# Optimization experiments

Hardware: AMD Instinct MI355X
Metric: run time of the kernel (lower is better)

## Reference

```python
import jax, jax.numpy as jnp
import numpy as np

DRUG_DIM, PROT_DIM, HIDDEN_DIM, OUTPUT_DIM = 128, 128, 256, 256


def setup_inputs() -> dict:
    key = jax.random.key(0)
    ks = jax.random.split(key, 7)
    B, n_d, n_p = 8, 64, 1024
    s = lambda d: 1.0 / np.sqrt(d)
    return {
        "X_d": jax.random.normal(ks[0], (B, n_d, DRUG_DIM), dtype=jnp.float32),
        "X_p": jax.random.normal(ks[1], (B, n_p, PROT_DIM), dtype=jnp.float32),
        # nn.Linear(in, out) weights have shape (out, in); we store transposed (in, out)
        "W_d": jax.random.uniform(ks[2], (DRUG_DIM, HIDDEN_DIM), jnp.float32, -s(DRUG_DIM), s(DRUG_DIM)),
        "W_p": jax.random.uniform(ks[3], (PROT_DIM, HIDDEN_DIM), jnp.float32, -s(PROT_DIM), s(PROT_DIM)),
        "W_a": jax.random.uniform(ks[4], (DRUG_DIM, OUTPUT_DIM), jnp.float32, -s(DRUG_DIM), s(DRUG_DIM)),
        "W_b": jax.random.uniform(ks[5], (PROT_DIM, OUTPUT_DIM), jnp.float32, -s(PROT_DIM), s(PROT_DIM)),
        "w_score": jax.random.uniform(ks[6], (HIDDEN_DIM,), jnp.float32, -s(HIDDEN_DIM), s(HIDDEN_DIM)),
    }


def reference(X_d, X_p, W_d, W_p, W_a, W_b, w_score):
    # Projections: (B, n_d, H), (B, n_p, H), (B, n_d, O), (B, n_p, O)
    hd = jnp.einsum("bik,kh->bih", X_d, W_d)
    hp = jnp.einsum("bjk,kh->bjh", X_p, W_p)
    fd = jnp.einsum("bik,ko->bio", X_d, W_a)
    fp = jnp.einsum("bjk,ko->bjo", X_p, W_b)

    # N_ij = tanh(hd_i + hp_j): (B, n_d, n_p, H); scores = N @ w_score
    N = jnp.tanh(hd[:, :, None, :] + hp[:, None, :, :])
    scores = jnp.einsum("bijh,h->bij", N, w_score)
    A = jax.nn.softmax(scores, axis=-1)  # softmax over protein dim

    # f_ij = tanh(fd_i + fp_j): (B, n_d, n_p, O)
    f = jnp.tanh(fd[:, :, None, :] + fp[:, None, :, :])
    X_int = jnp.einsum("bij,bijo->bo", A, f)  # sum over i and j
    return X_int
```

## Files before the change

### kernel.cpp

```cpp
#include <hip/hip_runtime.h>

#define NB   8
#define ND   64
#define NP   1024
#define KDIM 128
#define HID  256
#define OUTD 256
#define CSC  2.885390081777927f
#define PSTR 1048

typedef __attribute__((ext_vector_type(8))) short  bf16x8;
typedef __attribute__((ext_vector_type(4))) float  f32x4;


__device__ __forceinline__ ushort f2bf(float f) {
    unsigned u = __float_as_uint(f);
    return (ushort)((u + 0x7FFFu + ((u >> 16) & 1u)) >> 16);
}

__global__ __launch_bounds__(256) void k_cast(
    const float* __restrict__ Xd, const float* __restrict__ Xp,
    const float* __restrict__ Wd, const float* __restrict__ Wa,
    const float* __restrict__ Wp, const float* __restrict__ Wb,
    ushort* __restrict__ Xdbf, ushort* __restrict__ Xpbf,
    ushort* __restrict__ WdT, ushort* __restrict__ WaT,
    ushort* __restrict__ WpT, ushort* __restrict__ WbT) {
    int blk = blockIdx.x, t = threadIdx.x;
    if (blk < 1024) {
        size_t i = ((size_t)blk << 10) + ((size_t)t << 2);
        float4 v = *(const float4*)(Xp + i);
        ushort4 o; o.x = f2bf(v.x); o.y = f2bf(v.y); o.z = f2bf(v.z); o.w = f2bf(v.w);
        *(ushort4*)(Xpbf + i) = o;
    } else if (blk < 1088) {
        size_t i = ((size_t)(blk - 1024) << 10) + ((size_t)t << 2);
        float4 v = *(const float4*)(Xd + i);
        ushort4 o; o.x = f2bf(v.x); o.y = f2bf(v.y); o.z = f2bf(v.z); o.w = f2bf(v.w);
        *(ushort4*)(Xdbf + i) = o;
    } else {
        int r = blk - 1088, mat = r >> 5;
        const float* W = (mat == 0) ? Wd : (mat == 1) ? Wa : (mat == 2) ? Wp : Wb;
        ushort* WT = (mat == 0) ? WdT : (mat == 1) ? WaT : (mat == 2) ? WpT : WbT;
        int o0 = ((r & 31) << 10) + (t << 2);
        int n = o0 >> 7, k0 = o0 & 127;
        ushort4 o;
        o.x = f2bf(W[(k0 + 0) * HID + n]);
        o.y = f2bf(W[(k0 + 1) * HID + n]);
        o.z = f2bf(W[(k0 + 2) * HID + n]);
        o.w = f2bf(W[(k0 + 3) * HID + n]);
        *(ushort4*)(WT + o0) = o;
    }
}

__global__ __launch_bounds__(256) void k_proj_mfma(
    const ushort* __restrict__ Xpbf, const ushort* __restrict__ Xdbf,
    const ushort* __restrict__ WdT, const ushort* __restrict__ WaT,
    const ushort* __restrict__ WpT, const ushort* __restrict__ WbT,
    float* __restrict__ Ehd, float* __restrict__ Efd,
    float* __restrict__ EhpT, float* __restrict__ Efp) {
    int blk = blockIdx.x, t = threadIdx.x;
    const ushort *A, *B;
    float* out; size_t obase; int ostride, am0, bn0;
    if (blk < 512) {
        int mt = blk >> 2, nt = blk & 3;
        A = Xpbf; am0 = mt * 64; B = WbT; bn0 = nt * 64;
        out = Efp; obase = (size_t)am0 * HID + bn0; ostride = HID;
    } else if (blk < 1024) {
        int r = blk - 512, b = r >> 6, rr = r & 63;
        int mt = rr >> 4, nt = rr & 15;
        A = WpT; am0 = mt * 64;
        B = Xpbf + (size_t)b * NP * KDIM; bn0 = nt * 64;
        out = EhpT; obase = ((size_t)(b * 256 + am0)) * NP + bn0; ostride = NP;
    } else if (blk < 1056) {
        int r = blk - 1024; int mt = r >> 2, nt = r & 3;
        A = Xdbf; am0 = mt * 64; B = WdT; bn0 = nt * 64;
        out = Ehd; obase = (size_t)am0 * HID + bn0; ostride = HID;
    } else {
        int r = blk - 1056; int mt = r >> 2, nt = r & 3;
        A = Xdbf; am0 = mt * 64; B = WaT; bn0 = nt * 64;
        out = Efd; obase = (size_t)am0 * HID + bn0; ostride = HID;
    }
    int l = t & 63, w = t >> 6;
    int wm = (w >> 1) << 5, wn = (w & 1) << 5;
    int lr = l & 15, lk = (l >> 4) << 3;
    const ushort* Ab = A + (size_t)(am0 + wm + lr) * KDIM + lk;
    const ushort* Bb = B + (size_t)(bn0 + wn + lr) * KDIM + lk;

    bf16x8 af[2][4], bfr[2][4];
#pragma unroll
    for (int f = 0; f < 2; ++f)
#pragma unroll
        for (int ks = 0; ks < 4; ++ks) {
            af[f][ks]  = *(const bf16x8*)(Ab + (size_t)(f << 4) * KDIM + (ks << 5));
            bfr[f][ks] = *(const bf16x8*)(Bb + (size_t)(f << 4) * KDIM + (ks << 5));
        }

    f32x4 acc[2][2];
#pragma unroll
    for (int mf = 0; mf < 2; ++mf)
#pragma unroll
        for (int nf = 0; nf < 2; ++nf) acc[mf][nf] = (f32x4){0.f, 0.f, 0.f, 0.f};
#pragma unroll
    for (int ks = 0; ks < 4; ++ks)
#pragma unroll
        for (int mf = 0; mf < 2; ++mf)
#pragma unroll
            for (int nf = 0; nf < 2; ++nf)
                acc[mf][nf] = __builtin_amdgcn_mfma_f32_16x16x32_bf16(
                    af[mf][ks], bfr[nf][ks], acc[mf][nf], 0, 0, 0);

#pragma unroll
    for (int mf = 0; mf < 2; ++mf)
#pragma unroll
        for (int nf = 0; nf < 2; ++nf)
#pragma unroll
            for (int r = 0; r < 4; ++r) {
                int m = wm + (mf << 4) + ((l >> 4) << 2) + r;
                int n = wn + (nf << 4) + (l & 15);
                out[obase + (size_t)m * ostride + n] =
                    __builtin_amdgcn_exp2f(acc[mf][nf][r] * CSC);
            }
}

__global__ __launch_bounds__(1024) void k_fused(
    const float* __restrict__ Ehd, const float* __restrict__ EhpT,
    const float* __restrict__ Efd, const float* __restrict__ Efp,
    const float* __restrict__ wsc, float* __restrict__ part) {
    int blk = blockIdx.x;
    int b = blk & 7, pair = blk >> 3;
    int row0 = b * ND + pair * 2;
    int t = threadIdx.x;

    __shared__ float2 hrow[256];
    __shared__ float  w2s[256];
    __shared__ float2 a2[1024];
    __shared__ float  sred[8 * PSTR];
    __shared__ float  wsum0[16], wsum1[16];

    if (t < 256) {
        hrow[t] = make_float2(Ehd[((size_t)row0 << 8) + t],
                              Ehd[((size_t)(row0 + 1) << 8) + t]);
        w2s[t] = -2.0f * wsc[t];
    }
    __syncthreads();

    {
        int jq = t & 255, hq = t >> 8;
        const float* pB = EhpT + ((size_t)((b << 8) + (hq << 6))) * NP + (jq << 2);
        float a00 = 0, a01 = 0, a02 = 0, a03 = 0;
        float a10 = 0, a11 = 0, a12 = 0, a13 = 0;
        float4 pc = *(const float4*)(pB);
        float4 pn = *(const float4*)(pB + NP);
#pragma unroll
        for (int hh = 0; hh < 64; ++hh) {
            float4 pf = pc;
            if (hh + 2 < 64) pf = *(const float4*)(pB + (size_t)(hh + 2) * NP);
            int h = (hq << 6) + hh;
            float2 hv = hrow[h];
            float wv = w2s[h];
            a00 = fmaf(wv, __builtin_amdgcn_rcpf(fmaf(hv.x, pc.x, 1.f)), a00);
            a01 = fmaf(wv, __builtin_amdgcn_rcpf(fmaf(hv.x, pc.y, 1.f)), a01);
            a02 = fmaf(wv, __builtin_amdgcn_rcpf(fmaf(hv.x, pc.z, 1.f)), a02);
            a03 = fmaf(wv, __builtin_amdgcn_rcpf(fmaf(hv.x, pc.w, 1.f)), a03);
            a10 = fmaf(wv, __builtin_amdgcn_rcpf(fmaf(hv.y, pc.x, 1.f)), a10);
            a11 = fmaf(wv, __builtin_amdgcn_rcpf(fmaf(hv.y, pc.y, 1.f)), a11);
            a12 = fmaf(wv, __builtin_amdgcn_rcpf(fmaf(hv.y, pc.z, 1.f)), a12);
            a13 = fmaf(wv, __builtin_amdgcn_rcpf(fmaf(hv.y, pc.w, 1.f)), a13);
            pc = pn; pn = pf;
        }
        int base = (hq << 8) + jq;
        sred[0 * PSTR + base] = a00;  sred[1 * PSTR + base] = a01;
        sred[2 * PSTR + base] = a02;  sred[3 * PSTR + base] = a03;
        sred[4 * PSTR + base] = a10;  sred[5 * PSTR + base] = a11;
        sred[6 * PSTR + base] = a12;  sred[7 * PSTR + base] = a13;
    }
    __syncthreads();

    {
        int jq2 = t >> 2, c = t & 3;
        const float* p0 = sred + c * PSTR + jq2;
        const float* p1 = sred + (4 + c) * PSTR + jq2;
        float sc0 = (p0[0] + p0[256]) + (p0[512] + p0[768]);
        float sc1 = (p1[0] + p1[256]) + (p1[512] + p1[768]);
        const float L2E = 1.4426950408889634f;
        float e0 = __builtin_amdgcn_exp2f(sc0 * L2E);
        float e1 = __builtin_amdgcn_exp2f(sc1 * L2E);
        float s0 = e0, s1 = e1;
#pragma unroll
        for (int off = 32; off > 0; off >>= 1) {
            s0 += __shfl_xor(s0, off, 64);
            s1 += __shfl_xor(s1, off, 64);
        }
        if ((t & 63) == 0) { wsum0[t >> 6] = s0; wsum1[t >> 6] = s1; }
        __syncthreads();
        float tot0 = 0.f, tot1 = 0.f;
#pragma unroll
        for (int w = 0; w < 16; ++w) { tot0 += wsum0[w]; tot1 += wsum1[w]; }
        float sn0 = -2.0f * __builtin_amdgcn_rcpf(tot0);
        float sn1 = -2.0f * __builtin_amdgcn_rcpf(tot1);
        a2[t] = make_float2(e0 * sn0, e1 * sn1);
    }
    __syncthreads();

    {
        int oq = t & 63, jg = t >> 6;
        int o0 = oq << 2;
        float4 fd0 = *(const float4*)(Efd + ((size_t)row0 << 8) + o0);
        float4 fd1 = *(const float4*)(Efd + ((size_t)(row0 + 1) << 8) + o0);
        const float* fpB = Efp + ((size_t)(b * NP + (jg << 6)) << 8) + o0;
        float b00 = 0, b01 = 0, b02 = 0, b03 = 0;
        float b10 = 0, b11 = 0, b12 = 0, b13 = 0;
        float4 fc = *(const float4*)(fpB);
        float4 fn = *(const float4*)(fpB + 256);
#pragma unroll
        for (int jj = 0; jj < 64; ++jj) {
            float4 ff = fc;
            if (jj + 2 < 64) ff = *(const float4*)(fpB + ((size_t)(jj + 2) << 8));
            float2 av = a2[(jg << 6) + jj];
            b00 = fmaf(av.x, __builtin_amdgcn_rcpf(fmaf(fd0.x, fc.x, 1.f)), b00);
            b01 = fmaf(av.x, __builtin_amdgcn_rcpf(fmaf(fd0.y, fc.y, 1.f)), b01);
            b02 = fmaf(av.x, __builtin_amdgcn_rcpf(fmaf(fd0.z, fc.z, 1.f)), b02);
            b03 = fmaf(av.x, __builtin_amdgcn_rcpf(fmaf(fd0.w, fc.w, 1.f)), b03);
            b10 = fmaf(av.y, __builtin_amdgcn_rcpf(fmaf(fd1.x, fc.x, 1.f)), b10);
            b11 = fmaf(av.y, __builtin_amdgcn_rcpf(fmaf(fd1.y, fc.y, 1.f)), b11);
            b12 = fmaf(av.y, __builtin_amdgcn_rcpf(fmaf(fd1.z, fc.z, 1.f)), b12);
            b13 = fmaf(av.y, __builtin_amdgcn_rcpf(fmaf(fd1.w, fc.w, 1.f)), b13);
            fc = fn; fn = ff;
        }
        __syncthreads();
        int base = (jg << 6) + oq;
        sred[0 * PSTR + base] = b00;  sred[1 * PSTR + base] = b01;
        sred[2 * PSTR + base] = b02;  sred[3 * PSTR + base] = b03;
        sred[4 * PSTR + base] = b10;  sred[5 * PSTR + base] = b11;
        sred[6 * PSTR + base] = b12;  sred[7 * PSTR + base] = b13;
    }
    __syncthreads();

    if (t < 512) {
        int r = t >> 8, o = t & 255;
        int oq2 = o >> 2, c2 = o & 3;
        const float* pk = sred + (r * 4 + c2) * PSTR + oq2;
        float s = 0.f;
#pragma unroll
        for (int g = 0; g < 16; ++g) s += pk[g << 6];
        part[((size_t)((b << 6) + (pair << 1) + r) << 8) + o] = s;
    }
}

__global__ __launch_bounds__(256) void k_reduce(
    const float* __restrict__ part, float* __restrict__ out) {
    int b = blockIdx.x, t = threadIdx.x;
    float s = 64.0f;
#pragma unroll 8
    for (int i = 0; i < 64; ++i)
        s += part[((size_t)((b << 6) + i) << 8) + t];
    out[(b << 8) + t] = s;
}

extern "C" void kernel_launch(void* const* d_in, const int* in_sizes, int n_in,
                              void* d_out, int out_size, void* d_ws, size_t ws_size,
                              hipStream_t stream) {
    const float* Xd  = (const float*)d_in[0];
    const float* Xp  = (const float*)d_in[1];
    const float* Wd  = (const float*)d_in[2];
    const float* Wp  = (const float*)d_in[3];
    const float* Wa  = (const float*)d_in[4];
    const float* Wb  = (const float*)d_in[5];
    const float* wsc = (const float*)d_in[6];
    float* out = (float*)d_out;

    float* ws = (float*)d_ws;
    float* Ehd  = ws;
    float* Efd  = Ehd + NB * ND * HID;
    float* EhpT = Efd + NB * ND * OUTD;
    float* Efp  = EhpT + NB * NP * HID;
    float* stage = Efp + NB * NP * OUTD;
    ushort* Xpbf = (ushort*)stage;
    ushort* Xdbf = Xpbf + NB * NP * KDIM;
    ushort* WdT  = Xdbf + 65536;
    ushort* WaT  = WdT + 32768;
    ushort* WpT  = WaT + 32768;
    ushort* WbT  = WpT + 32768;
    float* part  = stage;

    k_cast     <<<1216, 256, 0, stream>>>(Xd, Xp, Wd, Wa, Wp, Wb,
                                          Xdbf, Xpbf, WdT, WaT, WpT, WbT);
    k_proj_mfma<<<1088, 256, 0, stream>>>(Xpbf, Xdbf, WdT, WaT, WpT, WbT,
                                          Ehd, Efd, EhpT, Efp);
    k_fused    <<<256, 1024, 0, stream>>>(Ehd, EhpT, Efd, Efp, wsc, part);
    k_reduce   <<<NB, 256, 0, stream>>>(part, out);
}
```

Baseline: 63.41 us.

## Stage hp/fp tiles into LDS with double-buffered async global_load_lds

Both main loops in the fused kernel now copy 32 KB chunks of the transposed hp and the fp projections into a two-slot LDS buffer using global_load_lds, instead of each thread streaming its own global loads through registers. While one chunk is being computed on, the next is prefetched, and the hd row and score weight are packed into one float4 table. The aim is to hide global/L2 latency and take load traffic out of the register file. In exchange it adds 64 extra block barriers, about 64 KB more LDS, and depends on the compiler inserting correct waits for the async LDS loads.

```diff
diff --git a/kernel.cpp b/kernel.cpp
--- a/kernel.cpp
+++ b/kernel.cpp
@@ -17,6 +17,10 @@
     unsigned u = __float_as_uint(f);
     return (ushort)((u + 0x7FFFu + ((u >> 16) & 1u)) >> 16);
 }
+
+#define GLD16(g, l) __builtin_amdgcn_global_load_lds(                        \
+    (const __attribute__((address_space(1))) void*)(g),                      \
+    (__attribute__((address_space(3))) void*)(l), 16, 0, 0)
 
 __global__ __launch_bounds__(256) void k_cast(
     const float* __restrict__ Xd, const float* __restrict__ Xp,
@@ -130,49 +134,59 @@
     int row0 = b * ND + pair * 2;
     int t = threadIdx.x;
 
-    __shared__ float2 hrow[256];
-    __shared__ float  w2s[256];
+    __shared__ float  ebuf[2][8192];
+    __shared__ float4 hw4[256];
     __shared__ float2 a2[1024];
     __shared__ float  sred[8 * PSTR];
     __shared__ float  wsum0[16], wsum1[16];
 
-    if (t < 256) {
-        hrow[t] = make_float2(Ehd[((size_t)row0 << 8) + t],
-                              Ehd[((size_t)(row0 + 1) << 8) + t]);
-        w2s[t] = -2.0f * wsc[t];
-    }
+    if (t < 256)
+        hw4[t] = make_float4(Ehd[((size_t)row0 << 8) + t],
+                             Ehd[((size_t)(row0 + 1) << 8) + t],
+                             -2.0f * wsc[t], 0.f);
+
+    const float* Eb = EhpT + ((size_t)(b << 8)) * NP;
+    const float* Fb = Efp + ((size_t)(b * NP)) * 256;
+
+#define STAGE(dst, gbase)                                                    \
+    do {                                                                     \
+        GLD16((gbase) + (t << 2),        &ebuf[dst][(t << 2)]);              \
+        GLD16((gbase) + 4096 + (t << 2), &ebuf[dst][4096 + (t << 2)]);       \
+    } while (0)
+
+    STAGE(0, Eb);
     __syncthreads();
 
+    float a00 = 0, a01 = 0, a02 = 0, a03 = 0;
+    float a10 = 0, a11 = 0, a12 = 0, a13 = 0;
+    int jq = t & 255, rep = t >> 8;
+    for (int c = 0; c < 32; ++c) {
+        if (c < 31) STAGE((c + 1) & 1, Eb + ((size_t)(c + 1) << 13));
+        const float* eb = ebuf[c & 1];
+#pragma unroll
+        for (int hl = 0; hl < 2; ++hl) {
+            int hloc = rep + (hl << 2);
+            float4 hw = hw4[(c << 3) + hloc];
+            float4 p = *(const float4*)(eb + (hloc << 10) + (jq << 2));
+            a00 = fmaf(hw.z, __builtin_amdgcn_rcpf(fmaf(hw.x, p.x, 1.f)), a00);
+            a01 = fmaf(hw.z, __builtin_amdgcn_rcpf(fmaf(hw.x, p.y, 1.f)), a01);
+            a02 = fmaf(hw.z, __builtin_amdgcn_rcpf(fmaf(hw.x, p.z, 1.f)), a02);
+            a03 = fmaf(hw.z, __builtin_amdgcn_rcpf(fmaf(hw.x, p.w, 1.f)), a03);
+            a10 = fmaf(hw.z, __builtin_amdgcn_rcpf(fmaf(hw.y, p.x, 1.f)), a10);
+            a11 = fmaf(hw.z, __builtin_amdgcn_rcpf(fmaf(hw.y, p.y, 1.f)), a11);
+            a12 = fmaf(hw.z, __builtin_amdgcn_rcpf(fmaf(hw.y, p.z, 1.f)), a12);
+            a13 = fmaf(hw.z, __builtin_amdgcn_rcpf(fmaf(hw.y, p.w, 1.f)), a13);
+        }
+        __syncthreads();
+    }
     {
-        int jq = t & 255, hq = t >> 8;
-        const float* pB = EhpT + ((size_t)((b << 8) + (hq << 6))) * NP + (jq << 2);
-        float a00 = 0, a01 = 0, a02 = 0, a03 = 0;
-        float a10 = 0, a11 = 0, a12 = 0, a13 = 0;
-        float4 pc = *(const float4*)(pB);
-        float4 pn = *(const float4*)(pB + NP);
-#pragma unroll
-        for (int hh = 0; hh < 64; ++hh) {
-            float4 pf = pc;
-            if (hh + 2 < 64) pf = *(const float4*)(pB + (size_t)(hh + 2) * NP);
-            int h = (hq << 6) + hh;
-            float2 hv = hrow[h];
-            float wv = w2s[h];
-            a00 = fmaf(wv, __builtin_amdgcn_rcpf(fmaf(hv.x, pc.x, 1.f)), a00);
-            a01 = fmaf(wv, __builtin_amdgcn_rcpf(fmaf(hv.x, pc.y, 1.f)), a01);
-            a02 = fmaf(wv, __builtin_amdgcn_rcpf(fmaf(hv.x, pc.z, 1.f)), a02);
-            a03 = fmaf(wv, __builtin_amdgcn_rcpf(fmaf(hv.x, pc.w, 1.f)), a03);
-            a10 = fmaf(wv, __builtin_amdgcn_rcpf(fmaf(hv.y, pc.x, 1.f)), a10);
-            a11 = fmaf(wv, __builtin_amdgcn_rcpf(fmaf(hv.y, pc.y, 1.f)), a11);
-            a12 = fmaf(wv, __builtin_amdgcn_rcpf(fmaf(hv.y, pc.z, 1.f)), a12);
-            a13 = fmaf(wv, __builtin_amdgcn_rcpf(fmaf(hv.y, pc.w, 1.f)), a13);
-            pc = pn; pn = pf;
-        }
-        int base = (hq << 8) + jq;
+        int base = (rep << 8) + jq;
         sred[0 * PSTR + base] = a00;  sred[1 * PSTR + base] = a01;
         sred[2 * PSTR + base] = a02;  sred[3 * PSTR + base] = a03;
         sred[4 * PSTR + base] = a10;  sred[5 * PSTR + base] = a11;
         sred[6 * PSTR + base] = a12;  sred[7 * PSTR + base] = a13;
     }
+    STAGE(0, Fb);
     __syncthreads();
 
     {
@@ -201,33 +215,33 @@
     }
     __syncthreads();
 
-    {
-        int oq = t & 63, jg = t >> 6;
-        int o0 = oq << 2;
-        float4 fd0 = *(const float4*)(Efd + ((size_t)row0 << 8) + o0);
-        float4 fd1 = *(const float4*)(Efd + ((size_t)(row0 + 1) << 8) + o0);
-        const float* fpB = Efp + ((size_t)(b * NP + (jg << 6)) << 8) + o0;
-        float b00 = 0, b01 = 0, b02 = 0, b03 = 0;
-        float b10 = 0, b11 = 0, b12 = 0, b13 = 0;
-        float4 fc = *(const float4*)(fpB);
-        float4 fn = *(const float4*)(fpB + 256);
-#pragma unroll
-        for (int jj = 0; jj < 64; ++jj) {
-            float4 ff = fc;
-            if (jj + 2 < 64) ff = *(const float4*)(fpB + ((size_t)(jj + 2) << 8));
-            float2 av = a2[(jg << 6) + jj];
-            b00 = fmaf(av.x, __builtin_amdgcn_rcpf(fmaf(fd0.x, fc.x, 1.f)), b00);
-            b01 = fmaf(av.x, __builtin_amdgcn_rcpf(fmaf(fd0.y, fc.y, 1.f)), b01);
-            b02 = fmaf(av.x, __builtin_amdgcn_rcpf(fmaf(fd0.z, fc.z, 1.f)), b02);
-            b03 = fmaf(av.x, __builtin_amdgcn_rcpf(fmaf(fd0.w, fc.w, 1.f)), b03);
-            b10 = fmaf(av.y, __builtin_amdgcn_rcpf(fmaf(fd1.x, fc.x, 1.f)), b10);
-            b11 = fmaf(av.y, __builtin_amdgcn_rcpf(fmaf(fd1.y, fc.y, 1.f)), b11);
-            b12 = fmaf(av.y, __builtin_amdgcn_rcpf(fmaf(fd1.z, fc.z, 1.f)), b12);
-            b13 = fmaf(av.y, __builtin_amdgcn_rcpf(fmaf(fd1.w, fc.w, 1.f)), b13);
-            fc = fn; fn = ff;
+    float b00 = 0, b01 = 0, b02 = 0, b03 = 0;
+    float b10 = 0, b11 = 0, b12 = 0, b13 = 0;
+    int oq = t & 63, wv = t >> 6;
+    int o0 = oq << 2;
+    float4 fd0 = *(const float4*)(Efd + ((size_t)row0 << 8) + o0);
+    float4 fd1 = *(const float4*)(Efd + ((size_t)(row0 + 1) << 8) + o0);
+    for (int c = 0; c < 32; ++c) {
+        if (c < 31) STAGE((c + 1) & 1, Fb + ((size_t)(c + 1) << 13));
+        const float* eb = ebuf[c & 1];
+#pragma unroll
+        for (int jl = 0; jl < 2; ++jl) {
+            int jloc = wv + (jl << 4);
+            float2 av = a2[(c << 5) + jloc];
+            float4 f = *(const float4*)(eb + (jloc << 8) + o0);
+            b00 = fmaf(av.x, __builtin_amdgcn_rcpf(fmaf(fd0.x, f.x, 1.f)), b00);
+            b01 = fmaf(av.x, __builtin_amdgcn_rcpf(fmaf(fd0.y, f.y, 1.f)), b01);
+            b02 = fmaf(av.x, __builtin_amdgcn_rcpf(fmaf(fd0.z, f.z, 1.f)), b02);
+            b03 = fmaf(av.x, __builtin_amdgcn_rcpf(fmaf(fd0.w, f.w, 1.f)), b03);
+            b10 = fmaf(av.y, __builtin_amdgcn_rcpf(fmaf(fd1.x, f.x, 1.f)), b10);
+            b11 = fmaf(av.y, __builtin_amdgcn_rcpf(fmaf(fd1.y, f.y, 1.f)), b11);
+            b12 = fmaf(av.y, __builtin_amdgcn_rcpf(fmaf(fd1.z, f.z, 1.f)), b12);
+            b13 = fmaf(av.y, __builtin_amdgcn_rcpf(fmaf(fd1.w, f.w, 1.f)), b13);
         }
         __syncthreads();
-        int base = (jg << 6) + oq;
+    }
+    {
+        int base = (wv << 6) + oq;
         sred[0 * PSTR + base] = b00;  sred[1 * PSTR + base] = b01;
         sred[2 * PSTR + base] = b02;  sred[3 * PSTR + base] = b03;
         sred[4 * PSTR + base] = b10;  sred[5 * PSTR + base] = b11;
@@ -244,6 +258,7 @@
         for (int g = 0; g < 16; ++g) s += pk[g << 6];
         part[((size_t)((b << 6) + (pair << 1) + r) << 8) + o] = s;
     }
+#undef STAGE
 }
 
 __global__ __launch_bounds__(256) void k_reduce(
```

Measured after the change: 86.32 us. 36.1% more time.
